# Kernel tuning notes

Hardware: AMD Instinct MI355X
Metric: run time of the kernel (lower is better)

Reference implementation:

```python
import jax, jax.numpy as jnp
import numpy as np

MD = 20          # max_displacement
TEMP = 1e-4      # softmax temperature
B, C, H, W = 4, 64, 112, 112


def setup_inputs() -> dict:
    key = jax.random.key(0)
    k1, k2 = jax.random.split(key)
    in1 = jax.random.normal(k1, (B, C, H, W), dtype=jnp.float32)
    in2 = jax.random.normal(k2, (B, C, H, W), dtype=jnp.float32)
    return {"in1": in1, "in2": in2}


def reference(in1, in2):
    b, c, h, w = in1.shape
    # F.normalize(x, dim=1): x / max(||x||_2, eps)
    def l2n(x):
        return x / jnp.maximum(jnp.linalg.norm(x, axis=1, keepdims=True), 1e-12)
    in1 = l2n(in1)
    in2 = l2n(in2)

    pad = jnp.pad(in2, ((0, 0), (0, 0), (MD, MD), (MD, MD)))

    d = jnp.arange(-MD, MD + 1)
    dx, dy = jnp.meshgrid(d, d, indexing="ij")  # torch.meshgrid default 'ij'
    dx = dx.reshape(-1)  # [K] with K = (2*MD+1)^2
    dy = dy.reshape(-1)

    def sim_one(dxi, dyi):
        # shifted window of padded in2, same spatial size as in1
        sl = jax.lax.dynamic_slice(pad, (0, 0, MD + dxi, MD + dyi), (b, c, h, w))
        return jnp.sum(in1 * sl, axis=1)  # [B,H,W]

    sim = jax.vmap(sim_one)(dx, dy)          # [K,B,H,W]
    sim = jnp.transpose(sim, (1, 0, 2, 3))   # [B,K,H,W] cost volume

    weights = jax.nn.softmax(sim / TEMP, axis=1)  # softmax over displacements
    guide = jnp.stack((dx, dy), axis=-1).astype(jnp.float32)  # [K,2]
    # flow[b,d,h,w] = sum_k weights[b,k,h,w] * guide[k,d]
    flow = jnp.einsum("bkhw,kd->bdhw", weights, guide)
    return flow
```

## Files before the change

### kernel.cpp

```cpp
#include <hip/hip_runtime.h>

#define BB 4
#define CC 64
#define HH 112
#define WW 112
#define MD 20
#define KD 41
#define S2 14426.950408f
#define NPIX (BB*HH*WW)
#define NT 10
#define ROW2 (NT*2*2*64*8)
#define IN2S_BYTES ((size_t)BB*HH*ROW2*2)
#define NEG (-60000.0f)

typedef _Float16 half8   __attribute__((ext_vector_type(8)));
typedef float    f32x4   __attribute__((ext_vector_type(4)));
typedef unsigned short ushort8 __attribute__((ext_vector_type(8)));

static __device__ __forceinline__ float fmax_f(float a, float b) { return a > b ? a : b; }
static __device__ __forceinline__ unsigned short f2h_bits(float x) {
    _Float16 h = (_Float16)x;
    return __builtin_bit_cast(unsigned short, h);
}
static __device__ __forceinline__ float h2f(unsigned short s) {
    return (float)__builtin_bit_cast(_Float16, s);
}
static __device__ __forceinline__ f32x4 vmax4(f32x4 a, f32x4 b) {
    f32x4 r;
    #pragma unroll
    for (int k = 0; k < 4; ++k) r[k] = a[k] > b[k] ? a[k] : b[k];
    return r;
}
static __device__ __forceinline__ f32x4 vexp4(f32x4 d) {
    f32x4 r;
    #pragma unroll
    for (int k = 0; k < 4; ++k) r[k] = __builtin_amdgcn_exp2f(d[k]);
    return r;
}
static __device__ __forceinline__ f32x4 mfma16(half8 a, half8 b, f32x4 c) {
    return __builtin_amdgcn_mfma_f32_16x16x32_f16(a, b, c, 0, 0, 0);
}

__global__ __launch_bounds__(64) void pack_kernel(const float* __restrict__ in2,
                                                  unsigned short* __restrict__ in2s) {
    int wid = blockIdx.x;
    int lane = threadIdx.x;
    int tau = wid % NT;
    int bh  = wid / NT;
    int b = bh / HH, h = bh % HH;
    int n = lane & 15, q = lane >> 4;
    int col = 16*tau + n - MD;
    bool ok = (col >= 0 && col < WW);
    const float* src = in2 + ((size_t)(b*CC)*HH + h)*WW + (ok ? col : 0);

    float x[16];
    float ss = 0.f;
    #pragma unroll
    for (int ks = 0; ks < 2; ++ks)
        #pragma unroll
        for (int j = 0; j < 8; ++j) {
            float v = ok ? src[(size_t)(32*ks + 8*q + j)*(HH*WW)] : 0.f;
            x[ks*8 + j] = v;
            ss += v*v;
        }
    ss += __shfl_xor(ss, 16);
    ss += __shfl_xor(ss, 32);
    float iv = 1.0f / fmax_f(__builtin_sqrtf(ss), 1e-12f);

    unsigned short* base = in2s + (size_t)(b*HH + h)*ROW2;
    #pragma unroll
    for (int ks = 0; ks < 2; ++ks) {
        ushort8 hb, lb;
        #pragma unroll
        for (int j = 0; j < 8; ++j) {
            float v = x[ks*8 + j] * iv;
            unsigned short vh = f2h_bits(v);
            hb[j] = vh;
            lb[j] = f2h_bits((v - h2f(vh)) * 4096.0f);
        }
        *(ushort8*)(base + (size_t)((tau*4 + ks*2 + 0)*64 + lane)*8) = hb;
        *(ushort8*)(base + (size_t)((tau*4 + ks*2 + 1)*64 + lane)*8) = lb;
    }
}

template<int TN, int NQ>
static __device__ __forceinline__ void corr_tiles(int b, int h, int g, int q0, int lane,
                                                  const float* __restrict__ in1,
                                                  const unsigned short* __restrict__ in2s,
                                                  float* __restrict__ part) {
    int n = lane & 15, q = lane >> 4;
    int m0 = 4*q;

    half8 aH[TN][2], aL[TN][2];
    #pragma unroll
    for (int t = 0; t < TN; ++t) {
        int wA = (q0 + t)*16 + n;
        const float* a_src = in1 + ((size_t)(b*CC)*HH + h)*WW + wA;
        float x[16], ss = 0.f;
        #pragma unroll
        for (int ks = 0; ks < 2; ++ks)
            #pragma unroll
            for (int j = 0; j < 8; ++j) {
                float v = a_src[(size_t)(32*ks + 8*q + j)*(HH*WW)];
                x[ks*8 + j] = v;
                ss += v*v;
            }
        ss += __shfl_xor(ss, 16);
        ss += __shfl_xor(ss, 32);
        float i1 = 1.0f / fmax_f(__builtin_sqrtf(ss), 1e-12f);
        #pragma unroll
        for (int ks = 0; ks < 2; ++ks)
            #pragma unroll
            for (int j = 0; j < 8; ++j) {
                float v = x[ks*8 + j] * i1;
                _Float16 vh = (_Float16)v;
                aH[t][ks][j] = vh;
                aL[t][ks][j] = (_Float16)((v - (float)vh) * 4096.0f);
            }
    }

    f32x4 NM20; bool v0b[4], v2b[4], v3b[4];
    #pragma unroll
    for (int r = 0; r < 4; ++r) {
        int nm = n - (m0 + r);
        NM20[r] = (float)(nm - 20);
        v0b[r] = (nm >= 0);
        v2b[r] = (nm <= 8);
        v3b[r] = (nm <= -8);
    }

    f32x4 SM[TN], SL[TN], SSX[TN], SSY[TN];
    #pragma unroll
    for (int t = 0; t < TN; ++t) {
        SM[t] = f32x4{NEG,NEG,NEG,NEG}; SL[t] = f32x4{0.f,0.f,0.f,0.f};
        SSX[t] = f32x4{0.f,0.f,0.f,0.f}; SSY[t] = f32x4{0.f,0.f,0.f,0.f};
    }

    int glo = g*14;
    int ghi = glo + 14 < KD ? glo + 14 : KD;
    int lo = glo > (MD - h) ? glo : (MD - h);
    int hi0 = HH + MD - h;
    int hi = ghi < hi0 ? ghi : hi0;
    if (hi < lo) { lo = ghi; hi = ghi; }

    for (int dxi = lo; dxi < hi; ++dxi) {
        const unsigned short* rb = in2s + (size_t)(b*HH + (h + dxi - MD))*ROW2
                                 + (size_t)q0*2048 + (size_t)lane*8;
        half8 bq[NQ][4];
        #pragma unroll
        for (int j = 0; j < NQ; ++j) {
            const half8* fp = (const half8*)(rb + (size_t)j*2048);
            bq[j][0] = fp[0];
            bq[j][1] = fp[64];
            bq[j][2] = fp[128];
            bq[j][3] = fp[192];
        }
        float dxf = (float)(dxi - MD);
        #pragma unroll
        for (int t = 0; t < TN; ++t) {
            f32x4 sv[4];
            #pragma unroll
            for (int oi = 0; oi < 4; ++oi) {
                const half8* f = bq[t + oi];
                f32x4 a0 = {0.f,0.f,0.f,0.f}, a1 = {0.f,0.f,0.f,0.f};
                a0 = mfma16(aH[t][0], f[0], a0);
                a1 = mfma16(aH[t][0], f[1], a1);
                a1 = mfma16(aL[t][0], f[0], a1);
                a0 = mfma16(aH[t][1], f[2], a0);
                a1 = mfma16(aH[t][1], f[3], a1);
                a1 = mfma16(aL[t][1], f[2], a1);
                sv[oi] = a0*S2 + a1*(S2/4096.0f);
            }
            f32x4 V0, V1 = sv[1], V2, V3;
            #pragma unroll
            for (int r = 0; r < 4; ++r) {
                V0[r] = v0b[r] ? sv[0][r] : NEG;
                V2[r] = v2b[r] ? sv[2][r] : NEG;
                V3[r] = v3b[r] ? sv[3][r] : NEG;
            }
            f32x4 MN = vmax4(vmax4(SM[t], V0), vmax4(V1, vmax4(V2, V3)));
            f32x4 ER = vexp4(SM[t] - MN);
            f32x4 E0 = vexp4(V0 - MN);
            f32x4 E1 = vexp4(V1 - MN);
            f32x4 E2 = vexp4(V2 - MN);
            f32x4 E3 = vexp4(V3 - MN);
            f32x4 SUM = (E0 + E1) + (E2 + E3);
            f32x4 TT  = E1 + E2*2.0f + E3*3.0f;
            SL[t]  = SL[t] *ER + SUM;
            SSX[t] = SSX[t]*ER + SUM*dxf;
            SSY[t] = SSY[t]*ER + (TT*16.0f + NM20*SUM);
            SM[t]  = MN;
        }
    }

    int miss = (lo - glo) + (ghi - hi);
    if (miss > 0) {
        float sdx = 0.f;
        for (int d = glo; d < lo; ++d)  sdx += (float)(d - MD);
        for (int d = hi; d < ghi; ++d)  sdx += (float)(d - MD);
        float cntf = (float)miss * (float)KD;
        #pragma unroll
        for (int t = 0; t < TN; ++t) {
            f32x4 Z = {0.f,0.f,0.f,0.f};
            f32x4 MN = vmax4(SM[t], Z);
            f32x4 ER = vexp4(SM[t] - MN);
            f32x4 E0 = vexp4(Z - MN);
            SL[t]  = SL[t] *ER + E0*cntf;
            SSX[t] = SSX[t]*ER + E0*((float)KD*sdx);
            SSY[t] = SSY[t]*ER;
            SM[t]  = MN;
        }
    }

    #pragma unroll
    for (int t = 0; t < TN; ++t) {
        #pragma unroll
        for (int off = 1; off < 16; off <<= 1) {
            f32x4 M2, L2, X2, Y2;
            #pragma unroll
            for (int k = 0; k < 4; ++k) {
                M2[k] = __shfl_xor(SM[t][k],  off);
                L2[k] = __shfl_xor(SL[t][k],  off);
                X2[k] = __shfl_xor(SSX[t][k], off);
                Y2[k] = __shfl_xor(SSY[t][k], off);
            }
            f32x4 MN = vmax4(SM[t], M2);
            f32x4 EA = vexp4(SM[t] - MN);
            f32x4 EB = vexp4(M2 - MN);
            SL[t]  = SL[t] *EA + L2*EB;
            SSX[t] = SSX[t]*EA + X2*EB;
            SSY[t] = SSY[t]*EA + Y2*EB;
            SM[t]  = MN;
        }
        if (n == 0) {
            #pragma unroll
            for (int r = 0; r < 4; ++r) {
                int w = (q0 + t)*16 + m0 + r;
                int pix = (b*HH + h)*WW + w;
                f32x4 rec = {SM[t][r], SL[t][r], SSX[t][r], SSY[t][r]};
                *(f32x4*)&part[(size_t)(g*NPIX + pix)*4] = rec;
            }
        }
    }
}

__global__ __launch_bounds__(256, 2) void corr_kernel(const float* __restrict__ in1,
                                                      const unsigned short* __restrict__ in2s,
                                                      float* __restrict__ part) {
    int gid = blockIdx.x;
    int xcd  = gid & 7;
    int slot = gid >> 3;
    int hloc = slot % 56;
    int g    = slot / 56;
    int b    = xcd >> 1;
    int h    = (xcd & 1)*56 + hloc;
    int u    = threadIdx.x >> 6;
    int lane = threadIdx.x & 63;

    if (u < 3) corr_tiles<2,5>(b, h, g, 2*u, lane, in1, in2s, part);
    else       corr_tiles<1,4>(b, h, g, 6,   lane, in1, in2s, part);
}

__global__ __launch_bounds__(256) void merge_kernel(const float* __restrict__ part,
                                                    float* __restrict__ out) {
    int idx = blockIdx.x*256 + threadIdx.x;
    if (idx >= NPIX) return;
    const float* p0 = &part[(size_t)idx*4];
    const float* p1 = &part[(size_t)(NPIX + idx)*4];
    const float* p2 = &part[(size_t)(2*NPIX + idx)*4];
    float M = fmax_f(fmax_f(p0[0], p1[0]), p2[0]);
    float e0 = __builtin_amdgcn_exp2f(p0[0] - M);
    float e1 = __builtin_amdgcn_exp2f(p1[0] - M);
    float e2 = __builtin_amdgcn_exp2f(p2[0] - M);
    float L  = p0[1]*e0 + p1[1]*e1 + p2[1]*e2;
    float SX = p0[2]*e0 + p1[2]*e1 + p2[2]*e2;
    float SY = p0[3]*e0 + p1[3]*e1 + p2[3]*e2;
    int b = idx / (HH*WW), rem = idx % (HH*WW);
    out[(b*2 + 0)*(HH*WW) + rem] = SX / L;
    out[(b*2 + 1)*(HH*WW) + rem] = SY / L;
}

extern "C" void kernel_launch(void* const* d_in, const int* in_sizes, int n_in,
                              void* d_out, int out_size, void* d_ws, size_t ws_size,
                              hipStream_t stream) {
    const float* in1 = (const float*)d_in[0];
    const float* in2 = (const float*)d_in[1];
    float* out = (float*)d_out;
    unsigned short* in2s = (unsigned short*)d_ws;
    float* part = (float*)((char*)d_ws + IN2S_BYTES);

    pack_kernel <<<BB*HH*NT, 64, 0, stream>>>(in2, in2s);
    corr_kernel <<<1344, 256, 0, stream>>>(in1, in2s, part);
    merge_kernel<<<(NPIX+255)/256, 256, 0, stream>>>(part, out);
}
```

Measured before the change: 155.0 us.

## Skip negligible softmax updates and split displacement range into six groups

Adds a per-tile running max that is shared across lanes with xor-shuffles. A whole tile's exp and accumulate update is skipped when every candidate score lies more than a fixed log2 margin below that max, since such terms contribute essentially nothing to the softmax. The displacement rows are split into six groups of seven instead of three of fourteen, which doubles the grid; launch bounds now ask for four blocks per CU, and the merge kernel combines six partials. The trade-offs are extra shuffle work, possible wave divergence on the skip branch, and register pressure from the tighter occupancy target.

```diff
diff --git a/kernel.cpp b/kernel.cpp
--- a/kernel.cpp
+++ b/kernel.cpp
@@ -12,6 +12,9 @@
 #define ROW2 (NT*2*2*64*8)
 #define IN2S_BYTES ((size_t)BB*HH*ROW2*2)
 #define NEG (-60000.0f)
+#define NG 6
+#define GSZ 7
+#define SKIP_MARGIN 40.0f
 
 typedef _Float16 half8   __attribute__((ext_vector_type(8)));
 typedef float    f32x4   __attribute__((ext_vector_type(4)));
@@ -129,15 +132,16 @@
         v3b[r] = (nm <= -8);
     }
 
-    f32x4 SM[TN], SL[TN], SSX[TN], SSY[TN];
+    f32x4 SM[TN], SL[TN], SSX[TN], SSY[TN], PM[TN];
     #pragma unroll
     for (int t = 0; t < TN; ++t) {
         SM[t] = f32x4{NEG,NEG,NEG,NEG}; SL[t] = f32x4{0.f,0.f,0.f,0.f};
         SSX[t] = f32x4{0.f,0.f,0.f,0.f}; SSY[t] = f32x4{0.f,0.f,0.f,0.f};
-    }
-
-    int glo = g*14;
-    int ghi = glo + 14 < KD ? glo + 14 : KD;
+        PM[t] = f32x4{NEG,NEG,NEG,NEG};
+    }
+
+    int glo = g*GSZ;
+    int ghi = glo + GSZ < KD ? glo + GSZ : KD;
     int lo = glo > (MD - h) ? glo : (MD - h);
     int hi0 = HH + MD - h;
     int hi = ghi < hi0 ? ghi : hi0;
@@ -178,18 +182,32 @@
                 V2[r] = v2b[r] ? sv[2][r] : NEG;
                 V3[r] = v3b[r] ? sv[3][r] : NEG;
             }
-            f32x4 MN = vmax4(vmax4(SM[t], V0), vmax4(V1, vmax4(V2, V3)));
-            f32x4 ER = vexp4(SM[t] - MN);
-            f32x4 E0 = vexp4(V0 - MN);
-            f32x4 E1 = vexp4(V1 - MN);
-            f32x4 E2 = vexp4(V2 - MN);
-            f32x4 E3 = vexp4(V3 - MN);
-            f32x4 SUM = (E0 + E1) + (E2 + E3);
-            f32x4 TT  = E1 + E2*2.0f + E3*3.0f;
-            SL[t]  = SL[t] *ER + SUM;
-            SSX[t] = SSX[t]*ER + SUM*dxf;
-            SSY[t] = SSY[t]*ER + (TT*16.0f + NM20*SUM);
-            SM[t]  = MN;
+            f32x4 mx = vmax4(vmax4(V0, V1), vmax4(V2, V3));
+            f32x4 d  = mx - PM[t];
+            float tm = fmax_f(fmax_f(d[0], d[1]), fmax_f(d[2], d[3]));
+            if (__any(tm > -SKIP_MARGIN)) {
+                f32x4 MN = vmax4(SM[t], mx);
+                f32x4 ER = vexp4(SM[t] - MN);
+                f32x4 E0 = vexp4(V0 - MN);
+                f32x4 E1 = vexp4(V1 - MN);
+                f32x4 E2 = vexp4(V2 - MN);
+                f32x4 E3 = vexp4(V3 - MN);
+                f32x4 SUM = (E0 + E1) + (E2 + E3);
+                f32x4 TT  = E1 + E2*2.0f + E3*3.0f;
+                SL[t]  = SL[t] *ER + SUM;
+                SSX[t] = SSX[t]*ER + SUM*dxf;
+                SSY[t] = SSY[t]*ER + (TT*16.0f + NM20*SUM);
+                SM[t]  = MN;
+                f32x4 pm = SM[t];
+                #pragma unroll
+                for (int off = 1; off < 16; off <<= 1) {
+                    f32x4 p2;
+                    #pragma unroll
+                    for (int k = 0; k < 4; ++k) p2[k] = __shfl_xor(pm[k], off);
+                    pm = vmax4(pm, p2);
+                }
+                PM[t] = pm;
+            }
         }
     }
 
@@ -244,7 +262,7 @@
     }
 }
 
-__global__ __launch_bounds__(256, 2) void corr_kernel(const float* __restrict__ in1,
+__global__ __launch_bounds__(256, 4) void corr_kernel(const float* __restrict__ in1,
                                                       const unsigned short* __restrict__ in2s,
                                                       float* __restrict__ part) {
     int gid = blockIdx.x;
@@ -265,16 +283,19 @@
                                                     float* __restrict__ out) {
     int idx = blockIdx.x*256 + threadIdx.x;
     if (idx >= NPIX) return;
-    const float* p0 = &part[(size_t)idx*4];
-    const float* p1 = &part[(size_t)(NPIX + idx)*4];
-    const float* p2 = &part[(size_t)(2*NPIX + idx)*4];
-    float M = fmax_f(fmax_f(p0[0], p1[0]), p2[0]);
-    float e0 = __builtin_amdgcn_exp2f(p0[0] - M);
-    float e1 = __builtin_amdgcn_exp2f(p1[0] - M);
-    float e2 = __builtin_amdgcn_exp2f(p2[0] - M);
-    float L  = p0[1]*e0 + p1[1]*e1 + p2[1]*e2;
-    float SX = p0[2]*e0 + p1[2]*e1 + p2[2]*e2;
-    float SY = p0[3]*e0 + p1[3]*e1 + p2[3]*e2;
+    float M = NEG;
+    #pragma unroll
+    for (int gg = 0; gg < NG; ++gg)
+        M = fmax_f(M, part[(size_t)(gg*NPIX + idx)*4]);
+    float L = 0.f, SX = 0.f, SY = 0.f;
+    #pragma unroll
+    for (int gg = 0; gg < NG; ++gg) {
+        const float* p = &part[(size_t)(gg*NPIX + idx)*4];
+        float e = __builtin_amdgcn_exp2f(p[0] - M);
+        L  += p[1]*e;
+        SX += p[2]*e;
+        SY += p[3]*e;
+    }
     int b = idx / (HH*WW), rem = idx % (HH*WW);
     out[(b*2 + 0)*(HH*WW) + rem] = SX / L;
     out[(b*2 + 1)*(HH*WW) + rem] = SY / L;
@@ -290,6 +311,6 @@
     float* part = (float*)((char*)d_ws + IN2S_BYTES);
 
     pack_kernel <<<BB*HH*NT, 64, 0, stream>>>(in2, in2s);
-    corr_kernel <<<1344, 256, 0, stream>>>(in1, in2s, part);
+    corr_kernel <<<8*56*NG, 256, 0, stream>>>(in1, in2s, part);
     merge_kernel<<<(NPIX+255)/256, 256, 0, stream>>>(part, out);
 }
```

Result: slower. 366.6 us (+136.5%).
